# Kernel tuning notes

Hardware: AMD Instinct MI355X
Metric: run time of the kernel (lower is better)

Reference implementation:

```python
import jax, jax.numpy as jnp
import numpy as np

N = 100000
E = 1600000
DIN = 128
H = 64
L = 2  # num_layer


def setup_inputs() -> dict:
    key = jax.random.key(0)
    ks = jax.random.split(key, 10)
    x = jax.random.normal(ks[0], (N, DIN), dtype=jnp.float32)
    edge_index = jax.random.randint(ks[1], (2, E), 0, N, dtype=jnp.int64)
    edge_attr = jax.random.uniform(ks[2], (E,), dtype=jnp.float32)
    batch = jnp.zeros((N,), dtype=jnp.int64)
    s_in = 1.0 / np.sqrt(DIN)
    s_h = 1.0 / np.sqrt(H)
    W_emb = jax.random.normal(ks[3], (DIN, H), dtype=jnp.float32) * s_in
    b_emb = jnp.zeros((H,), dtype=jnp.float32)
    # Stacked per-layer LEConv params: lin1 (W1,b1), lin2 (W2, no bias), lin3 (W3,b3)
    W1 = jax.random.normal(ks[4], (L, H, H), dtype=jnp.float32) * s_h
    b1 = jnp.zeros((L, H), dtype=jnp.float32)
    W2 = jax.random.normal(ks[5], (L, H, H), dtype=jnp.float32) * s_h
    W3 = jax.random.normal(ks[6], (L, H, H), dtype=jnp.float32) * s_h
    b3 = jnp.zeros((L, H), dtype=jnp.float32)
    return {"x": x, "edge_index": edge_index, "edge_attr": edge_attr, "batch": batch,
            "W_emb": W_emb, "b_emb": b_emb, "W1": W1, "b1": b1, "W2": W2,
            "W3": W3, "b3": b3}


def reference(x, edge_index, edge_attr, batch, W_emb, b_emb, W1, b1, W2, W3, b3):
    # node embedding
    h = x @ W_emb + b_emb  # [N, H]
    src = edge_index[0]  # message source j
    dst = edge_index[1]  # aggregation target i
    w = edge_attr[:, None]  # [E, 1]
    for l in range(L):
        a = h @ W1[l] + b1[l]          # lin1(x)
        b = h @ W2[l]                  # lin2(x), no bias
        # LEConv message: e_ji * (a_j - b_i), aggregated at i
        msg = (a[src] - b[dst]) * w    # [E, H]
        agg = jax.ops.segment_sum(msg, dst, num_segments=N)
        h = agg + h @ W3[l] + b3[l]    # + lin3(x)
        # dropout (eval mode => identity), then ReLU
        h = jax.nn.relu(h)
    return h
```

## Files before the change

### kernel.cpp

```cpp
#include <hip/hip_runtime.h>

#define NNODES 100000
#define NEDGES 1600000
#define DINP   128
#define HDIM   64
#define NLAYERS 2

#define NBUCK 256
#define BDIV  391
#define TILE  8192
#define NT    ((NEDGES + TILE - 1) / TILE)
#define NTOT  (NBUCK * NT)
#define SEG   (NTOT / 1024)
#define EMB_BLOCKS 1563

typedef unsigned short ushort_t;
typedef unsigned int   uint_t;
typedef unsigned char  uchar_t;
typedef __attribute__((ext_vector_type(8))) short bf16x8;
typedef __attribute__((ext_vector_type(4))) float f32x4;
typedef __attribute__((ext_vector_type(2))) float f32x2;

__device__ __forceinline__ ushort_t f32_to_bf16_rne(float x) {
    uint_t u = __float_as_uint(x);
    u = (u + 0x7FFFu + ((u >> 16) & 1u)) >> 16;
    return (ushort_t)u;
}
__device__ __forceinline__ float bf16_to_f32(ushort_t v) {
    return __uint_as_float(((uint_t)v) << 16);
}
__device__ __forceinline__ uint_t pack_bf16(float lo, float hi) {
    return (uint_t)f32_to_bf16_rne(lo) | ((uint_t)f32_to_bf16_rne(hi) << 16);
}


__global__ __launch_bounds__(256) void wprep_all(
    const float* __restrict__ Wemb, const float* __restrict__ W1,
    const float* __restrict__ W2, const float* __restrict__ W3,
    ushort_t* __restrict__ wefrag, ushort_t* __restrict__ wfrag)
{
    int t = blockIdx.x * 256 + threadIdx.x;
    if (t < 8192) {
        int j  = t & 7;
        int l  = (t >> 3) & 63;
        int nt = (t >> 9) & 3;
        int kb = (t >> 11) & 3;
        int k = kb * 32 + 8 * (l >> 4) + j;
        int n = nt * 16 + (l & 15);
        float w = Wemb[k * HDIM + n];
        ushort_t hi = f32_to_bf16_rne(w);
        ushort_t lo = f32_to_bf16_rne(w - bf16_to_f32(hi));
        wefrag[(((0 * 4 + kb) * 4 + nt) * 64 + l) * 8 + j] = hi;
        wefrag[(((1 * 4 + kb) * 4 + nt) * 64 + l) * 8 + j] = lo;
    } else {
        int u = t - 8192;
        if (u >= 2 * 3 * 2 * 4 * 64 * 8) return;
        int j    = u & 7;
        int l    = (u >> 3) & 63;
        int nt   = (u >> 9) & 3;
        int kb   = (u >> 11) & 1;
        int mat  = (u >> 12) % 3;
        int layer = u / 12288;
        int kp = kb * 32 + 8 * (l >> 4) + j;
        int k  = (kp & 3) * 16 + (kp >> 2);
        int n = nt * 16 + (l & 15);
        const float* Wm = (mat == 0) ? W1 : (mat == 1) ? W2 : W3;
        float w = Wm[(size_t)layer * HDIM * HDIM + k * HDIM + n];
        ushort_t hi = f32_to_bf16_rne(w);
        ushort_t lo = f32_to_bf16_rne(w - bf16_to_f32(hi));
        size_t base = (size_t)layer * 24576;
        wfrag[base + ((((size_t)(mat * 2 + 0) * 2 + kb) * 4 + nt) * 64 + l) * 8 + j] = hi;
        wfrag[base + ((((size_t)(mat * 2 + 1) * 2 + kb) * 4 + nt) * 64 + l) * 8 + j] = lo;
    }
}

__global__ __launch_bounds__(256) void emb_p1(
    const float* __restrict__ x, const ushort_t* __restrict__ wefrag,
    const float* __restrict__ bemb, ushort_t* __restrict__ hbf,
    uchar_t* __restrict__ hq8,
    const int* __restrict__ dst, int* __restrict__ tileOff)
{
    __shared__ int hist[NBUCK];
    if (blockIdx.x < EMB_BLOCKS) {
        const int wid = blockIdx.x * 4 + (threadIdx.x >> 6);
        if (wid >= NNODES / 16) return;
        const int lane = threadIdx.x & 63;
        const int lrow = lane & 15;
        const int lgrp = lane >> 4;
        const int r0 = wid * 16;

        f32x4 acc[4];
#pragma unroll
        for (int nt = 0; nt < 4; ++nt) acc[nt] = (f32x4){0.f, 0.f, 0.f, 0.f};

#pragma unroll
        for (int kb = 0; kb < 4; ++kb) {
            const float* xp = x + (size_t)(r0 + lrow) * DINP + kb * 32 + lgrp * 8;
            float4 xa = *(const float4*)xp;
            float4 xb = *(const float4*)(xp + 4);
            float xs[8] = {xa.x, xa.y, xa.z, xa.w, xb.x, xb.y, xb.z, xb.w};
            bf16x8 xhi, xlo;
#pragma unroll
            for (int q = 0; q < 8; ++q) {
                ushort_t hv = f32_to_bf16_rne(xs[q]);
                xhi[q] = (short)hv;
                xlo[q] = (short)f32_to_bf16_rne(xs[q] - bf16_to_f32(hv));
            }
#pragma unroll
            for (int nt = 0; nt < 4; ++nt) {
                bf16x8 bhi = *(const bf16x8*)(wefrag + (((0 * 4 + kb) * 4 + nt) * 64 + lane) * 8);
                bf16x8 blo = *(const bf16x8*)(wefrag + (((1 * 4 + kb) * 4 + nt) * 64 + lane) * 8);
                acc[nt] = __builtin_amdgcn_mfma_f32_16x16x32_bf16(xhi, bhi, acc[nt], 0, 0, 0);
                acc[nt] = __builtin_amdgcn_mfma_f32_16x16x32_bf16(xlo, bhi, acc[nt], 0, 0, 0);
                acc[nt] = __builtin_amdgcn_mfma_f32_16x16x32_bf16(xhi, blo, acc[nt], 0, 0, 0);
            }
        }

        float bv[4];
#pragma unroll
        for (int nt = 0; nt < 4; ++nt) bv[nt] = bemb[nt * 16 + lrow];

#pragma unroll
        for (int r = 0; r < 4; ++r) {
            int row = r0 + lgrp * 4 + r;
            float o[4];
#pragma unroll
            for (int nt = 0; nt < 4; ++nt) o[nt] = acc[nt][r] + bv[nt];
            uint2 hb;
            hb.x = pack_bf16(o[0], o[1]);
            hb.y = pack_bf16(o[2], o[3]);
            *(uint2*)(hbf + ((size_t)row << 6) + (lrow << 2)) = hb;
            int q = __builtin_amdgcn_cvt_pk_fp8_f32(o[0], o[1], 0, false);
            q = __builtin_amdgcn_cvt_pk_fp8_f32(o[2], o[3], q, true);
            *(int*)(hq8 + ((size_t)row << 6) + (lrow << 2)) = q;
        }
    } else {
        const int tl = blockIdx.x - EMB_BLOCKS, t = threadIdx.x;
        hist[t] = 0;
        __syncthreads();
        const int base = tl * TILE;
#pragma unroll
        for (int i = 0; i < TILE / 256; ++i) {
            int e = base + i * 256 + t;
            if (e < NEDGES) atomicAdd(&hist[dst[e] / BDIV], 1);
        }
        __syncthreads();
        tileOff[t * NT + tl] = hist[t];
    }
}

__global__ __launch_bounds__(1024) void p2_scan(int* __restrict__ tileOff)
{
    __shared__ int sd[1024];
    const int t = threadIdx.x;
    const int lo = t * SEG;
    int s = 0;
    for (int i = 0; i < SEG; ++i) s += tileOff[lo + i];
    sd[t] = s;
    __syncthreads();
    for (int off = 1; off < 1024; off <<= 1) {
        int v = (t >= off) ? sd[t - off] : 0;
        __syncthreads();
        sd[t] += v;
        __syncthreads();
    }
    int run = sd[t] - s;
    for (int i = 0; i < SEG; ++i) {
        int c = tileOff[lo + i];
        tileOff[lo + i] = run;
        run += c;
    }
}

__global__ __launch_bounds__(256) void p3_bin(
    const int* __restrict__ src, const int* __restrict__ dst,
    const float* __restrict__ attr, const int* __restrict__ tileOff,
    int2* __restrict__ tmp)
{
    __shared__ int cur[NBUCK];
    const int tl = blockIdx.x, t = threadIdx.x;
    cur[t] = tileOff[t * NT + tl];
    __syncthreads();
#pragma unroll
    for (int i = 0; i < TILE / 256; ++i) {
        int e = tl * TILE + i * 256 + t;
        if (e < NEDGES) {
            int d  = dst[e];
            int bk = d / BDIV;
            int ld = d - bk * BDIV;
            int pos = atomicAdd(&cur[bk], 1);
            int2 p;
            p.x = (ld << 17) | src[e];
            p.y = __float_as_int(attr[e]);
            tmp[pos] = p;
        }
    }
}

__global__ __launch_bounds__(256) void p4_sort(
    const int2* __restrict__ tmp, const int* __restrict__ tileOff,
    int2* __restrict__ edgeS, int* __restrict__ rowptr,
    float* __restrict__ degw)
{
    __shared__ int sdh[512];
    __shared__ int cur[BDIV + 1];
    __shared__ float sdw[BDIV];
    const int b = blockIdx.x, t = threadIdx.x;
    const int n0 = b * BDIV;
    const int nn = (NNODES - n0 < BDIV) ? (NNODES - n0) : BDIV;
    const int ebeg = tileOff[b * NT];
    const int eend = (b + 1 < NBUCK) ? tileOff[(b + 1) * NT] : NEDGES;

    sdh[t] = 0; sdh[t + 256] = 0;
    for (int i = t; i < BDIV; i += 256) sdw[i] = 0.f;
    __syncthreads();
    for (int e = ebeg + t; e < eend; e += 256)
        atomicAdd(&sdh[tmp[e].x >> 17], 1);
    __syncthreads();
    for (int off = 1; off < 512; off <<= 1) {
        int i0 = t, i1 = t + 256;
        int v0 = (i0 >= off) ? sdh[i0 - off] : 0;
        int v1 = (i1 >= off) ? sdh[i1 - off] : 0;
        __syncthreads();
        sdh[i0] += v0; sdh[i1] += v1;
        __syncthreads();
    }
    for (int i = t; i < nn; i += 256) {
        int c = ebeg + (i ? sdh[i - 1] : 0);
        cur[i] = c;
        rowptr[n0 + i] = c;
    }
    if (b == NBUCK - 1 && t == 0) rowptr[NNODES] = NEDGES;
    __syncthreads();
    for (int e = ebeg + t; e < eend; e += 256) {
        int2 w = tmp[e];
        int ld = w.x >> 17;
        int pos = atomicAdd(&cur[ld], 1);
        atomicAdd(&sdw[ld], __int_as_float(w.y));
        int2 p;
        p.x = (w.x & 0x1FFFF) << 6;
        p.y = w.y;
        edgeS[pos] = p;
    }
    __syncthreads();
    for (int i = t; i < nn; i += 256) degw[n0 + i] = sdw[i];
}

__global__ __launch_bounds__(256) void gather_kernel(
    const int* __restrict__ rowptr, const int2* __restrict__ edgeS,
    const uchar_t* __restrict__ hq8, ushort_t* __restrict__ aggbf)
{
    const int gid  = blockIdx.x * 256 + threadIdx.x;
    const int v    = gid >> 6;
    const int lane = threadIdx.x & 63;
    const int oct  = lane >> 3;
    const int ol   = lane & 7;
    const int beg = rowptr[v], end = rowptr[v + 1];
    const int cnt = end - beg;
    const uchar_t* __restrict__ hq8o = hq8 + (ol << 3);
    const int2* __restrict__ ep = edgeS + beg + oct;

    float a0 = 0.f, a1 = 0.f, a2 = 0.f, a3 = 0.f;
    float a4 = 0.f, a5 = 0.f, a6 = 0.f, a7 = 0.f;
    const int nfull = cnt >> 3;
#pragma unroll 2
    for (int k = 0; k < nfull; ++k) {
        int2 ev = ep[(size_t)k * 8];
        float wv = __int_as_float(ev.y);
        uint2 u = *(const uint2*)(hq8o + ev.x);
        f32x2 f01 = __builtin_amdgcn_cvt_pk_f32_fp8((int)u.x, false);
        f32x2 f23 = __builtin_amdgcn_cvt_pk_f32_fp8((int)u.x, true);
        f32x2 f45 = __builtin_amdgcn_cvt_pk_f32_fp8((int)u.y, false);
        f32x2 f67 = __builtin_amdgcn_cvt_pk_f32_fp8((int)u.y, true);
        a0 += wv * f01[0];  a1 += wv * f01[1];
        a2 += wv * f23[0];  a3 += wv * f23[1];
        a4 += wv * f45[0];  a5 += wv * f45[1];
        a6 += wv * f67[0];  a7 += wv * f67[1];
    }
    if (cnt & 7) {
        int idx = beg + (nfull << 3) + oct;
        bool ok = idx < end;
        int2 ev = edgeS[ok ? idx : beg];
        float wv = ok ? __int_as_float(ev.y) : 0.f;
        uint2 u = *(const uint2*)(hq8o + ev.x);
        f32x2 f01 = __builtin_amdgcn_cvt_pk_f32_fp8((int)u.x, false);
        f32x2 f23 = __builtin_amdgcn_cvt_pk_f32_fp8((int)u.x, true);
        f32x2 f45 = __builtin_amdgcn_cvt_pk_f32_fp8((int)u.y, false);
        f32x2 f67 = __builtin_amdgcn_cvt_pk_f32_fp8((int)u.y, true);
        a0 += wv * f01[0];  a1 += wv * f01[1];
        a2 += wv * f23[0];  a3 += wv * f23[1];
        a4 += wv * f45[0];  a5 += wv * f45[1];
        a6 += wv * f67[0];  a7 += wv * f67[1];
    }

    a0 += __shfl_xor(a0, 8); a0 += __shfl_xor(a0, 16); a0 += __shfl_xor(a0, 32);
    a1 += __shfl_xor(a1, 8); a1 += __shfl_xor(a1, 16); a1 += __shfl_xor(a1, 32);
    a2 += __shfl_xor(a2, 8); a2 += __shfl_xor(a2, 16); a2 += __shfl_xor(a2, 32);
    a3 += __shfl_xor(a3, 8); a3 += __shfl_xor(a3, 16); a3 += __shfl_xor(a3, 32);
    a4 += __shfl_xor(a4, 8); a4 += __shfl_xor(a4, 16); a4 += __shfl_xor(a4, 32);
    a5 += __shfl_xor(a5, 8); a5 += __shfl_xor(a5, 16); a5 += __shfl_xor(a5, 32);
    a6 += __shfl_xor(a6, 8); a6 += __shfl_xor(a6, 16); a6 += __shfl_xor(a6, 32);
    a7 += __shfl_xor(a7, 8); a7 += __shfl_xor(a7, 16); a7 += __shfl_xor(a7, 32);

    if (oct == 0) {
        uint4 o;
        o.x = pack_bf16(a0, a1);
        o.y = pack_bf16(a2, a3);
        o.z = pack_bf16(a4, a5);
        o.w = pack_bf16(a6, a7);
        *(uint4*)(aggbf + ((size_t)v << 6) + (ol << 3)) = o;
    }
}

template<int WRITE_BF>
__global__ __launch_bounds__(256) void dense_mfma(
    const ushort_t* __restrict__ hbf, const ushort_t* __restrict__ aggbf,
    const float* __restrict__ degw, const ushort_t* __restrict__ wfrag,
    const float* __restrict__ b1, const float* __restrict__ b3,
    float* __restrict__ hout, ushort_t* __restrict__ hbf_out,
    uchar_t* __restrict__ hq8_out)
{
    const int wid = blockIdx.x * 4 + (threadIdx.x >> 6);
    if (wid >= NNODES / 16) return;
    const int lane = threadIdx.x & 63;
    const int lrow = lane & 15;
    const int lgrp = lane >> 4;
    const int r0   = wid * 16;

    f32x4 acc[3][4];
#pragma unroll
    for (int m = 0; m < 3; ++m)
#pragma unroll
        for (int nt = 0; nt < 4; ++nt)
            acc[m][nt] = (f32x4){0.f, 0.f, 0.f, 0.f};

#pragma unroll
    for (int kb = 0; kb < 2; ++kb) {
        const size_t aoff = ((size_t)(r0 + lrow) << 6) + kb * 32 + lgrp * 8;
        bf16x8 a_agg = *(const bf16x8*)(aggbf + aoff);
        bf16x8 a_h   = *(const bf16x8*)(hbf + aoff);
#pragma unroll
        for (int mv = 0; mv < 6; ++mv) {
            const int mat = mv >> 1;
            bf16x8 a = (mat == 0) ? a_agg : a_h;
            const ushort_t* wb = wfrag + (((size_t)mv * 2 + kb) * 4) * 512 + lane * 8;
#pragma unroll
            for (int nt = 0; nt < 4; ++nt) {
                bf16x8 b = *(const bf16x8*)(wb + nt * 512);
                acc[mat][nt] = __builtin_amdgcn_mfma_f32_16x16x32_bf16(
                    a, b, acc[mat][nt], 0, 0, 0);
            }
        }
    }

    float dreg[4];
#pragma unroll
    for (int r = 0; r < 4; ++r) dreg[r] = degw[r0 + lgrp * 4 + r];

    float b1v[4], b3v[4];
#pragma unroll
    for (int nt = 0; nt < 4; ++nt) {
        b1v[nt] = b1[nt * 16 + lrow];
        b3v[nt] = b3[nt * 16 + lrow];
    }

#pragma unroll
    for (int r = 0; r < 4; ++r) {
        int row = r0 + lgrp * 4 + r;
        float o[4];
#pragma unroll
        for (int nt = 0; nt < 4; ++nt) {
            float t = acc[0][nt][r] + acc[2][nt][r] - dreg[r] * acc[1][nt][r]
                    + dreg[r] * b1v[nt] + b3v[nt];
            o[nt] = fmaxf(t, 0.f);
        }
        if (WRITE_BF) {
            uint2 hb;
            hb.x = pack_bf16(o[0], o[1]);
            hb.y = pack_bf16(o[2], o[3]);
            *(uint2*)(hbf_out + ((size_t)row << 6) + (lrow << 2)) = hb;
            int q = __builtin_amdgcn_cvt_pk_fp8_f32(o[0], o[1], 0, false);
            q = __builtin_amdgcn_cvt_pk_fp8_f32(o[2], o[3], q, true);
            *(int*)(hq8_out + ((size_t)row << 6) + (lrow << 2)) = q;
        } else {
#pragma unroll
            for (int nt = 0; nt < 4; ++nt)
                hout[((size_t)row << 6) + nt * 16 + lrow] = o[nt];
        }
    }
}

extern "C" void kernel_launch(void* const* d_in, const int* in_sizes, int n_in,
                              void* d_out, int out_size, void* d_ws, size_t ws_size,
                              hipStream_t stream)
{
    const float* x    = (const float*)d_in[0];
    const int*   eidx = (const int*)  d_in[1];
    const float* attr = (const float*)d_in[2];
    const float* Wemb = (const float*)d_in[4];
    const float* bemb = (const float*)d_in[5];
    const float* W1   = (const float*)d_in[6];
    const float* b1   = (const float*)d_in[7];
    const float* W2   = (const float*)d_in[8];
    const float* W3   = (const float*)d_in[9];
    const float* b3   = (const float*)d_in[10];

    float* hout = (float*)d_out;

    float*    degw    = (float*)d_ws;
    int*      rowptr  = (int*)d_ws + 100000;
    int*      tileOff = (int*)d_ws + 200016;
    int2*     edgeS   = (int2*)((int*)d_ws + 250192);
    ushort_t* hbf     = (ushort_t*)((int*)d_ws + 3450192);
    ushort_t* aggbf   = (ushort_t*)((int*)d_ws + 6650192);
    int2*     tmp     = (int2*)aggbf;
    ushort_t* wfrag   = (ushort_t*)((int*)d_ws + 9850192);
    ushort_t* wefrag  = (ushort_t*)((int*)d_ws + 9874768);
    uchar_t*  hq8     = (uchar_t*)((int*)d_ws + 9882960);

    const int* srcI = eidx;
    const int* dstI = eidx + NEDGES;

    wprep_all<<<128, 256, 0, stream>>>(Wemb, W1, W2, W3, wefrag, wfrag);

    emb_p1<<<EMB_BLOCKS + NT, 256, 0, stream>>>(
        x, wefrag, bemb, hbf, hq8, dstI, tileOff);

    p2_scan<<<1, 1024, 0, stream>>>(tileOff);
    p3_bin <<<NT, 256, 0, stream>>>(srcI, dstI, attr, tileOff, tmp);
    p4_sort<<<NBUCK, 256, 0, stream>>>(tmp, tileOff, edgeS, rowptr, degw);

    const int mfmaGrid = (NNODES / 16 + 3) / 4;
    gather_kernel<<<NNODES * HDIM / 256, 256, 0, stream>>>(
        rowptr, edgeS, hq8, aggbf);
    dense_mfma<1><<<mfmaGrid, 256, 0, stream>>>(
        hbf, aggbf, degw, wfrag, b1, b3, hout, hbf, hq8);
    gather_kernel<<<NNODES * HDIM / 256, 256, 0, stream>>>(
        rowptr, edgeS, hq8, aggbf);
    dense_mfma<0><<<mfmaGrid, 256, 0, stream>>>(
        hbf, aggbf, degw, wfrag + 24576, b1 + HDIM, b3 + HDIM, hout, hbf, hq8);
}
```

Before: 211.7 us.

## Use half-wave per node in gather and drop low-order x term in embedding

The gather kernel now assigns 32 threads per destination node instead of 64, with 4 edge slots per iteration instead of 8. This halves the grid and cuts one shuffle-reduction stage, aiming to reduce idle lanes given the average degree of about 16. The embedding GEMM also drops the xlo correction MFMA and its conversion work, lowering compute at the cost of precision in the embedding.

```diff
diff --git a/kernel.cpp b/kernel.cpp
--- a/kernel.cpp
+++ b/kernel.cpp
@@ -98,20 +98,20 @@
             const float* xp = x + (size_t)(r0 + lrow) * DINP + kb * 32 + lgrp * 8;
             float4 xa = *(const float4*)xp;
             float4 xb = *(const float4*)(xp + 4);
-            float xs[8] = {xa.x, xa.y, xa.z, xa.w, xb.x, xb.y, xb.z, xb.w};
-            bf16x8 xhi, xlo;
-#pragma unroll
-            for (int q = 0; q < 8; ++q) {
-                ushort_t hv = f32_to_bf16_rne(xs[q]);
-                xhi[q] = (short)hv;
-                xlo[q] = (short)f32_to_bf16_rne(xs[q] - bf16_to_f32(hv));
-            }
+            bf16x8 xhi;
+            xhi[0] = (short)f32_to_bf16_rne(xa.x);
+            xhi[1] = (short)f32_to_bf16_rne(xa.y);
+            xhi[2] = (short)f32_to_bf16_rne(xa.z);
+            xhi[3] = (short)f32_to_bf16_rne(xa.w);
+            xhi[4] = (short)f32_to_bf16_rne(xb.x);
+            xhi[5] = (short)f32_to_bf16_rne(xb.y);
+            xhi[6] = (short)f32_to_bf16_rne(xb.z);
+            xhi[7] = (short)f32_to_bf16_rne(xb.w);
 #pragma unroll
             for (int nt = 0; nt < 4; ++nt) {
                 bf16x8 bhi = *(const bf16x8*)(wefrag + (((0 * 4 + kb) * 4 + nt) * 64 + lane) * 8);
                 bf16x8 blo = *(const bf16x8*)(wefrag + (((1 * 4 + kb) * 4 + nt) * 64 + lane) * 8);
                 acc[nt] = __builtin_amdgcn_mfma_f32_16x16x32_bf16(xhi, bhi, acc[nt], 0, 0, 0);
-                acc[nt] = __builtin_amdgcn_mfma_f32_16x16x32_bf16(xlo, bhi, acc[nt], 0, 0, 0);
                 acc[nt] = __builtin_amdgcn_mfma_f32_16x16x32_bf16(xhi, blo, acc[nt], 0, 0, 0);
             }
         }
@@ -250,11 +250,10 @@
     const int* __restrict__ rowptr, const int2* __restrict__ edgeS,
     const uchar_t* __restrict__ hq8, ushort_t* __restrict__ aggbf)
 {
-    const int gid  = blockIdx.x * 256 + threadIdx.x;
-    const int v    = gid >> 6;
-    const int lane = threadIdx.x & 63;
-    const int oct  = lane >> 3;
-    const int ol   = lane & 7;
+    const int v   = blockIdx.x * 8 + (threadIdx.x >> 5);
+    const int t5  = threadIdx.x & 31;
+    const int oct = t5 >> 3;
+    const int ol  = t5 & 7;
     const int beg = rowptr[v], end = rowptr[v + 1];
     const int cnt = end - beg;
     const uchar_t* __restrict__ hq8o = hq8 + (ol << 3);
@@ -262,10 +261,10 @@
 
     float a0 = 0.f, a1 = 0.f, a2 = 0.f, a3 = 0.f;
     float a4 = 0.f, a5 = 0.f, a6 = 0.f, a7 = 0.f;
-    const int nfull = cnt >> 3;
+    const int nfull = cnt >> 2;
 #pragma unroll 2
     for (int k = 0; k < nfull; ++k) {
-        int2 ev = ep[(size_t)k * 8];
+        int2 ev = ep[(size_t)k * 4];
         float wv = __int_as_float(ev.y);
         uint2 u = *(const uint2*)(hq8o + ev.x);
         f32x2 f01 = __builtin_amdgcn_cvt_pk_f32_fp8((int)u.x, false);
@@ -277,8 +276,8 @@
         a4 += wv * f45[0];  a5 += wv * f45[1];
         a6 += wv * f67[0];  a7 += wv * f67[1];
     }
-    if (cnt & 7) {
-        int idx = beg + (nfull << 3) + oct;
+    if (cnt & 3) {
+        int idx = beg + (nfull << 2) + oct;
         bool ok = idx < end;
         int2 ev = edgeS[ok ? idx : beg];
         float wv = ok ? __int_as_float(ev.y) : 0.f;
@@ -293,14 +292,14 @@
         a6 += wv * f67[0];  a7 += wv * f67[1];
     }
 
-    a0 += __shfl_xor(a0, 8); a0 += __shfl_xor(a0, 16); a0 += __shfl_xor(a0, 32);
-    a1 += __shfl_xor(a1, 8); a1 += __shfl_xor(a1, 16); a1 += __shfl_xor(a1, 32);
-    a2 += __shfl_xor(a2, 8); a2 += __shfl_xor(a2, 16); a2 += __shfl_xor(a2, 32);
-    a3 += __shfl_xor(a3, 8); a3 += __shfl_xor(a3, 16); a3 += __shfl_xor(a3, 32);
-    a4 += __shfl_xor(a4, 8); a4 += __shfl_xor(a4, 16); a4 += __shfl_xor(a4, 32);
-    a5 += __shfl_xor(a5, 8); a5 += __shfl_xor(a5, 16); a5 += __shfl_xor(a5, 32);
-    a6 += __shfl_xor(a6, 8); a6 += __shfl_xor(a6, 16); a6 += __shfl_xor(a6, 32);
-    a7 += __shfl_xor(a7, 8); a7 += __shfl_xor(a7, 16); a7 += __shfl_xor(a7, 32);
+    a0 += __shfl_xor(a0, 8); a0 += __shfl_xor(a0, 16);
+    a1 += __shfl_xor(a1, 8); a1 += __shfl_xor(a1, 16);
+    a2 += __shfl_xor(a2, 8); a2 += __shfl_xor(a2, 16);
+    a3 += __shfl_xor(a3, 8); a3 += __shfl_xor(a3, 16);
+    a4 += __shfl_xor(a4, 8); a4 += __shfl_xor(a4, 16);
+    a5 += __shfl_xor(a5, 8); a5 += __shfl_xor(a5, 16);
+    a6 += __shfl_xor(a6, 8); a6 += __shfl_xor(a6, 16);
+    a7 += __shfl_xor(a7, 8); a7 += __shfl_xor(a7, 16);
 
     if (oct == 0) {
         uint4 o;
@@ -431,12 +430,11 @@
     p4_sort<<<NBUCK, 256, 0, stream>>>(tmp, tileOff, edgeS, rowptr, degw);
 
     const int mfmaGrid = (NNODES / 16 + 3) / 4;
-    gather_kernel<<<NNODES * HDIM / 256, 256, 0, stream>>>(
-        rowptr, edgeS, hq8, aggbf);
+    const int gatherGrid = NNODES / 8;
+    gather_kernel<<<gatherGrid, 256, 0, stream>>>(rowptr, edgeS, hq8, aggbf);
     dense_mfma<1><<<mfmaGrid, 256, 0, stream>>>(
         hbf, aggbf, degw, wfrag, b1, b3, hout, hbf, hq8);
-    gather_kernel<<<NNODES * HDIM / 256, 256, 0, stream>>>(
-        rowptr, edgeS, hq8, aggbf);
+    gather_kernel<<<gatherGrid, 256, 0, stream>>>(rowptr, edgeS, hq8, aggbf);
     dense_mfma<0><<<mfmaGrid, 256, 0, stream>>>(
         hbf, aggbf, degw, wfrag + 24576, b1 + HDIM, b3 + HDIM, hout, hbf, hq8);
 }
```

New measurement: 197.1 us. 1.07x faster.
